# Performance work log

Hardware: AMD Instinct MI355X
Metric: run time of the kernel (lower is better)

Reference implementation:

```python
import jax, jax.numpy as jnp
import numpy as np

DIM = 128
H = 4            # num_heads
HD = DIM // H    # head_dim = 32
NH = H // 2      # half heads
MAXD = 128       # rpe max_dist
SPAN = 2 * MAXD + 1
TABLE = SPAN * SPAN
LAMBDA_INIT = 0.8


def setup_inputs() -> dict:
    key = jax.random.key(0)
    ks = jax.random.split(key, 18)
    B, Nq, Nkv = 2, 2048, 4096
    n = jax.random.normal
    inp = {
        "x_q": n(ks[0], (B, Nq, DIM), dtype=jnp.float32),
        "x_kv": n(ks[1], (B, Nkv, DIM), dtype=jnp.float32),
        "coords_q": jax.random.randint(ks[2], (B, Nq, 2), 0, 256, dtype=jnp.int32),
        "coords_k": jax.random.randint(ks[3], (B, Nkv, 2), 0, 256, dtype=jnp.int32),
        "alpha_map": jax.random.uniform(ks[4], (B, Nq, 1), dtype=jnp.float32),
        # projection weights stored input-major: y = x @ W + b
        "Wq": n(ks[5], (DIM, DIM), dtype=jnp.float32) * 0.02,
        "bq": jnp.zeros((DIM,), jnp.float32),
        "Wk": n(ks[6], (DIM, DIM), dtype=jnp.float32) * 0.02,
        "bk": jnp.zeros((DIM,), jnp.float32),
        "Wv": n(ks[7], (DIM, DIM), dtype=jnp.float32) * 0.02,
        "bv": jnp.zeros((DIM,), jnp.float32),
        "lq1": n(ks[8], (NH, HD), dtype=jnp.float32) * 0.1,
        "lk1": n(ks[9], (NH, HD), dtype=jnp.float32) * 0.1,
        "lq2": n(ks[10], (NH, HD), dtype=jnp.float32) * 0.1,
        "lk2": n(ks[11], (NH, HD), dtype=jnp.float32) * 0.1,
        "rpe_table": n(ks[12], (TABLE, H), dtype=jnp.float32) * 0.02,
        "Wp": n(ks[13], (DIM, DIM), dtype=jnp.float32) * 0.02,
        "bp": jnp.zeros((DIM,), jnp.float32),
    }
    return inp


def reference(x_q, x_kv, coords_q, coords_k, alpha_map,
              Wq, bq, Wk, bk, Wv, bv,
              lq1, lk1, lq2, lk2, rpe_table, Wp, bp):
    B, Nq, C = x_q.shape
    Nkv = x_kv.shape[1]
    scale = HD ** -0.5

    def to_heads(x, W, b, n):
        return (x @ W + b).reshape(B, n, H, HD).transpose(0, 2, 1, 3)  # [B,H,n,hd]

    q = to_heads(x_q, Wq, bq, Nq)
    k = to_heads(x_kv, Wk, bk, Nkv)
    v = to_heads(x_kv, Wv, bv, Nkv)

    # relative position bias gather: [B,Nq,Nkv] indices into [TABLE,H]
    rel = coords_q[:, :, None, :] - coords_k[:, None, :, :] + MAXD
    rel = jnp.clip(rel, 0, 2 * MAXD)
    idx = rel[..., 0] * SPAN + rel[..., 1]
    bias = jnp.transpose(rpe_table[idx], (0, 3, 1, 2))  # [B,H,Nq,Nkv]

    scores = jnp.einsum('bhqd,bhkd->bhqk', q, k) * scale + bias
    probs = jax.nn.softmax(scores, axis=-1)
    x_std = jnp.einsum('bhqk,bhkd->bhqd', probs, v)

    lam = (jnp.exp(jnp.sum(lq1 * lk1, axis=-1))
           - jnp.exp(jnp.sum(lq2 * lk2, axis=-1)) + LAMBDA_INIT)  # [NH]
    attn_diff = probs[:, :NH] - lam[None, :, None, None] * probs[:, NH:]
    x_diff = jnp.einsum('bhqk,bhkd->bhqd', attn_diff, v[:, :NH])

    x1 = x_std[:, :NH] + alpha_map[:, None, :, :] * x_diff  # alpha gating
    x = jnp.concatenate([x1, x_std[:, NH:]], axis=1)        # [B,H,Nq,hd]
    x = x.transpose(0, 2, 1, 3).reshape(B, Nq, C)
    return x @ Wp + bp
```

## Files before the change

### kernel.cpp

```cpp
#include <hip/hip_runtime.h>
#include <hip/hip_bf16.h>

#define B_ 2
#define H_ 4
#define HD_ 32
#define NQ_ 2048
#define NKV_ 4096
#define DIM_ 128
#define SPAN_ 257
#define SCALE_ 0.17677669529663687f
#define LAMBDA_INIT_ 0.8f
#define DTHR 4.0f

typedef float f32x4 __attribute__((ext_vector_type(4)));
typedef short s16x4 __attribute__((ext_vector_type(4)));
typedef short s16x8 __attribute__((ext_vector_type(8)));
typedef int   i32x4 __attribute__((ext_vector_type(4)));
typedef float fl4   __attribute__((ext_vector_type(4)));

static __device__ __forceinline__ unsigned short f2bf(float f) {
  unsigned u = __float_as_uint(f);
  u += 0x7FFFu + ((u >> 16) & 1u);
  return (unsigned short)(u >> 16);
}
static __device__ __forceinline__ unsigned cvtpk(float lo, float hi) {
  unsigned r;
  asm("v_cvt_pk_bf16_f32 %0, %1, %2" : "=v"(r) : "v"(lo), "v"(hi));
  return r;
}

__global__ __launch_bounds__(128) void proj_q(const float* __restrict__ x,
    const float* __restrict__ W, const float* __restrict__ bias,
    unsigned short* __restrict__ out) {
  int row0 = blockIdx.x * 16;
  int b = row0 / NQ_, n0 = row0 % NQ_;
  __shared__ float xr[16][DIM_ + 1];
  int j = threadIdx.x;
#pragma unroll
  for (int r = 0; r < 16; ++r) xr[r][j] = x[(size_t)(row0 + r) * DIM_ + j];
  __syncthreads();
  float acc[16];
  float bb = bias[j];
#pragma unroll
  for (int r = 0; r < 16; ++r) acc[r] = bb;
#pragma unroll 4
  for (int i = 0; i < DIM_; ++i) {
    float w = W[i * DIM_ + j];
#pragma unroll
    for (int r = 0; r < 16; ++r) acc[r] = fmaf(xr[r][i], w, acc[r]);
  }
  int h = j >> 5, d = j & 31;
#pragma unroll
  for (int r = 0; r < 16; ++r)
    out[(((size_t)b * H_ + h) * NQ_ + n0 + r) * HD_ + d] = f2bf(acc[r]);
}

__global__ __launch_bounds__(256) void proj_kv(const float* __restrict__ x,
    const float* __restrict__ Wk, const float* __restrict__ bk,
    const float* __restrict__ Wv, const float* __restrict__ bv,
    unsigned short* __restrict__ Kb, unsigned short* __restrict__ Vsw) {
  int row0 = blockIdx.x * 16;
  int b = row0 / NKV_, n0 = row0 % NKV_;
  __shared__ float xr[16][DIM_ + 1];
  int tid = threadIdx.x;
  int half = tid >> 7, j = tid & 127;
#pragma unroll
  for (int c = 0; c < 8; ++c) {
    int e = tid + c * 256;
    xr[e >> 7][e & 127] = x[(size_t)row0 * DIM_ + e];
  }
  __syncthreads();
  const float* W = half ? Wv : Wk;
  float bb = half ? bv[j] : bk[j];
  float acc[16];
#pragma unroll
  for (int r = 0; r < 16; ++r) acc[r] = bb;
#pragma unroll 4
  for (int i = 0; i < DIM_; ++i) {
    float w = W[i * DIM_ + j];
#pragma unroll
    for (int r = 0; r < 16; ++r) acc[r] = fmaf(xr[r][i], w, acc[r]);
  }
  int h = j >> 5, d = j & 31;
  if (half == 0) {
#pragma unroll
    for (int r = 0; r < 16; ++r)
      Kb[(((size_t)b * H_ + h) * NKV_ + n0 + r) * HD_ + d] = f2bf(acc[r]);
  } else {
    size_t vrow = (((size_t)b * H_ + h) * HD_ + d) * NKV_ + (size_t)(n0 & ~31);
#pragma unroll
    for (int c = 0; c < 4; ++c) {
      int k0r = (n0 & 31) + 4 * c;
      int posb = (k0r < 16) ? 8 * (k0r >> 2) : 8 * ((k0r - 16) >> 2) + 4;
      s16x4 t4;
#pragma unroll
      for (int e = 0; e < 4; ++e) t4[e] = (short)f2bf(acc[4 * c + e]);
      *(s16x4*)(Vsw + vrow + posb) = t4;
    }
  }
}

__global__ __launch_bounds__(128) void proj_out(const float* __restrict__ x,
    const float* __restrict__ W, const float* __restrict__ bias,
    float* __restrict__ out) {
  int row0 = blockIdx.x * 16;
  __shared__ float xr[16][DIM_ + 1];
  int j = threadIdx.x;
#pragma unroll
  for (int r = 0; r < 16; ++r) xr[r][j] = x[(size_t)(row0 + r) * DIM_ + j];
  __syncthreads();
  float acc[16];
  float bb = bias[j];
#pragma unroll
  for (int r = 0; r < 16; ++r) acc[r] = bb;
#pragma unroll 4
  for (int i = 0; i < DIM_; ++i) {
    float w = W[i * DIM_ + j];
#pragma unroll
    for (int r = 0; r < 16; ++r) acc[r] = fmaf(xr[r][i], w, acc[r]);
  }
#pragma unroll
  for (int r = 0; r < 16; ++r) out[(size_t)(row0 + r) * DIM_ + j] = acc[r];
}

__global__ __launch_bounds__(512) void attn_nb(
    const unsigned short* __restrict__ Qg, const unsigned short* __restrict__ Kg,
    const unsigned short* __restrict__ Vg, const int* __restrict__ cq,
    const int* __restrict__ ck, const float* __restrict__ alpha,
    const float* __restrict__ rpe, const float* __restrict__ lq1,
    const float* __restrict__ lk1, const float* __restrict__ lq2,
    const float* __restrict__ lk2, float* __restrict__ xatt) {

  const int tid = threadIdx.x;
  const int lane = tid & 63;
  const int wv = tid >> 6;
  const int qcol = lane & 15;
  const int g = lane >> 4;
  const int qt = blockIdx.x & 127;
  const int b = blockIdx.x >> 7;
  const int qg0 = qt * 16;
  const int k_base = wv * 512;

  __shared__ struct {
    float acc[3][8][16][36];
    float mW[8][17];
    float lW[4][8][17];
    float wgt[8][17];
    float lam[2];
  } S;

  if (tid < 2) {
    float s1 = 0.f, s2 = 0.f;
    for (int d = 0; d < HD_; ++d) {
      s1 += lq1[tid * HD_ + d] * lk1[tid * HD_ + d];
      s2 += lq2[tid * HD_ + d] * lk2[tid * HD_ + d];
    }
    S.lam[tid] = __expf(s1) - __expf(s2) + LAMBDA_INIT_;
  }

  s16x8 qf[4];
#pragma unroll
  for (int h = 0; h < 4; ++h)
    qf[h] = *(const s16x8*)(Qg + (((size_t)b * H_ + h) * NQ_ + qg0 + qcol) * HD_ + 8 * g);

  const int2 cqv = ((const int2*)cq)[(size_t)b * NQ_ + qg0 + qcol];
  const int qx = cqv.x + 128, qy = cqv.y + 128;

  const unsigned short* kb[4];
  const unsigned short* vp[4][2];
#pragma unroll
  for (int h = 0; h < 4; ++h) {
    kb[h] = Kg + (((size_t)b * H_ + h) * NKV_ + k_base) * HD_;
#pragma unroll
    for (int dt = 0; dt < 2; ++dt)
      vp[h][dt] = Vg + (((size_t)b * H_ + h) * HD_ + dt * 16 + qcol) * NKV_ + k_base + 8 * g;
  }
  int koff[2];
#pragma unroll
  for (int t = 0; t < 2; ++t) koff[t] = (16 * t + qcol) * HD_ + 8 * g;

  const i32x4* ck4 = (const i32x4*)ck + (((size_t)b * NKV_ + k_base) >> 1);
  const fl4* __restrict__ rpe4 = (const fl4*)rpe;

  float m_run = -INFINITY;
  float l_run[4] = {0.f, 0.f, 0.f, 0.f};
  f32x4 z4 = {0.f, 0.f, 0.f, 0.f};
  f32x4 aS[4][2], aC[2][2];
#pragma unroll
  for (int h = 0; h < 4; ++h) { aS[h][0] = z4; aS[h][1] = z4; }
#pragma unroll
  for (int p = 0; p < 2; ++p) { aC[p][0] = z4; aC[p][1] = z4; }

  s16x8 kf[4][2], vf[4][2];
  i32x4 ckt[4];
  fl4 gB[8];

#define CKLD(ST) {                                                         \
    const int s_ = (ST);                                                   \
    _Pragma("unroll") for (int t = 0; t < 2; ++t)                          \
    _Pragma("unroll") for (int hf = 0; hf < 2; ++hf)                       \
      ckt[2 * t + hf] = ck4[s_ * 16 + 8 * t + 2 * g + hf];                 \
  }
#define KLD(ST) {                                                          \
    const int s_ = (ST);                                                   \
    _Pragma("unroll") for (int h = 0; h < 4; ++h)                          \
    _Pragma("unroll") for (int t = 0; t < 2; ++t)                          \
      kf[h][t] = *(const s16x8*)(kb[h] + s_ * 32 * HD_ + koff[t]);         \
  }
#define VLD(ST) {                                                          \
    const int s_ = (ST);                                                   \
    _Pragma("unroll") for (int h = 0; h < 4; ++h)                          \
    _Pragma("unroll") for (int dt = 0; dt < 2; ++dt)                       \
      vf[h][dt] = *(const s16x8*)(vp[h][dt] + s_ * 32);                    \
  }
#define GATH() {                                                           \
    _Pragma("unroll") for (int t = 0; t < 2; ++t)                          \
    _Pragma("unroll") for (int hf = 0; hf < 2; ++hf) {                     \
      i32x4 cc = ckt[2 * t + hf];                                          \
      int dx0 = qx - cc[0]; dx0 = dx0 < 0 ? 0 : (dx0 > 256 ? 256 : dx0);   \
      int dy0 = qy - cc[1]; dy0 = dy0 < 0 ? 0 : (dy0 > 256 ? 256 : dy0);   \
      gB[4 * t + 2 * hf] = rpe4[dx0 * SPAN_ + dy0];                        \
      int dx1 = qx - cc[2]; dx1 = dx1 < 0 ? 0 : (dx1 > 256 ? 256 : dx1);   \
      int dy1 = qy - cc[3]; dy1 = dy1 < 0 ? 0 : (dy1 > 256 ? 256 : dy1);   \
      gB[4 * t + 2 * hf + 1] = rpe4[dx1 * SPAN_ + dy1];                    \
    }                                                                      \
  }

  CKLD(0);
  KLD(0);
  GATH();
  CKLD(1);

  for (int st = 0; st < 16; ++st) {
    f32x4 s0[4], s1[4];
#pragma unroll
    for (int h = 0; h < 4; ++h) {
      s0[h] = __builtin_amdgcn_mfma_f32_16x16x32_bf16(kf[h][0], qf[h], z4, 0, 0, 0);
      s1[h] = __builtin_amdgcn_mfma_f32_16x16x32_bf16(kf[h][1], qf[h], z4, 0, 0, 0);
    }
    VLD(st);
    KLD(st + 1 < 16 ? st + 1 : 15);

    float sv[4][8];
    float mx = -INFINITY;
#pragma unroll
    for (int h = 0; h < 4; ++h) {
#pragma unroll
      for (int r = 0; r < 4; ++r) {
        sv[h][r]     = fmaf(s0[h][r], SCALE_, gB[r][h]);
        sv[h][4 + r] = fmaf(s1[h][r], SCALE_, gB[4 + r][h]);
        mx = fmaxf(mx, fmaxf(sv[h][r], sv[h][4 + r]));
      }
    }
    mx = fmaxf(mx, __shfl_xor(mx, 16));
    mx = fmaxf(mx, __shfl_xor(mx, 32));
    if (__any(mx > m_run + DTHR)) {
      float mnew = fmaxf(m_run, mx);
      float fold = __expf(m_run - mnew);
      float fr[4];
#pragma unroll
      for (int r = 0; r < 4; ++r) fr[r] = __shfl(fold, 4 * g + r);
#pragma unroll
      for (int h = 0; h < 4; ++h) {
        l_run[h] *= fold;
#pragma unroll
        for (int dt = 0; dt < 2; ++dt)
#pragma unroll
          for (int r = 0; r < 4; ++r) aS[h][dt][r] *= fr[r];
      }
#pragma unroll
      for (int p = 0; p < 2; ++p)
#pragma unroll
        for (int dt = 0; dt < 2; ++dt)
#pragma unroll
          for (int r = 0; r < 4; ++r) aC[p][dt][r] *= fr[r];
      m_run = mnew;
    }
    s16x8 pa[4];
#pragma unroll
    for (int h = 0; h < 4; ++h) {
      float p[8], psum = 0.f;
#pragma unroll
      for (int s = 0; s < 8; ++s) { p[s] = __expf(sv[h][s] - m_run); psum += p[s]; }
      l_run[h] += psum;
      i32x4 pw;
#pragma unroll
      for (int c = 0; c < 4; ++c) pw[c] = (int)cvtpk(p[2 * c], p[2 * c + 1]);
      pa[h] = __builtin_bit_cast(s16x8, pw);
    }
    GATH();
    CKLD(st + 2 < 16 ? st + 2 : 15);

#pragma unroll
    for (int h = 0; h < 4; ++h)
#pragma unroll
      for (int dt = 0; dt < 2; ++dt)
        aS[h][dt] = __builtin_amdgcn_mfma_f32_16x16x32_bf16(pa[h], vf[h][dt], aS[h][dt], 0, 0, 0);
#pragma unroll
    for (int p = 0; p < 2; ++p)
#pragma unroll
      for (int dt = 0; dt < 2; ++dt)
        aC[p][dt] = __builtin_amdgcn_mfma_f32_16x16x32_bf16(pa[p + 2], vf[p][dt], aC[p][dt], 0, 0, 0);
  }

#pragma unroll
  for (int h = 0; h < 4; ++h) {
    l_run[h] += __shfl_xor(l_run[h], 16);
    l_run[h] += __shfl_xor(l_run[h], 32);
  }
  if (lane < 16) {
    S.mW[wv][lane] = m_run;
#pragma unroll
    for (int h = 0; h < 4; ++h) S.lW[h][wv][lane] = l_run[h];
  }
  __syncthreads();
  if (tid < 128) {
    int w = tid >> 4, q = tid & 15;
    float M = -INFINITY;
#pragma unroll
    for (int w2 = 0; w2 < 8; ++w2) M = fmaxf(M, S.mW[w2][q]);
    S.wgt[w][q] = __expf(S.mW[w][q] - M);
  }
  __syncthreads();

#pragma unroll
  for (int p = 0; p < 3; ++p)
#pragma unroll
    for (int dt = 0; dt < 2; ++dt)
#pragma unroll
      for (int r = 0; r < 4; ++r)
        S.acc[p][wv][4 * g + r][dt * 16 + qcol] = aS[p][dt][r];
  __syncthreads();
  const int q = tid >> 5, d = tid & 31;
  float wg[8];
#pragma unroll
  for (int w = 0; w < 8; ++w) wg[w] = S.wgt[w][q];
  float sumA[3] = {0.f, 0.f, 0.f};
#pragma unroll
  for (int p = 0; p < 3; ++p)
#pragma unroll
    for (int w = 0; w < 8; ++w) sumA[p] = fmaf(wg[w], S.acc[p][w][q][d], sumA[p]);
  __syncthreads();

#pragma unroll
  for (int dt = 0; dt < 2; ++dt)
#pragma unroll
    for (int r = 0; r < 4; ++r) {
      S.acc[0][wv][4 * g + r][dt * 16 + qcol] = aS[3][dt][r];
      S.acc[1][wv][4 * g + r][dt * 16 + qcol] = aC[0][dt][r];
      S.acc[2][wv][4 * g + r][dt * 16 + qcol] = aC[1][dt][r];
    }
  __syncthreads();
  float sumB[3] = {0.f, 0.f, 0.f};
#pragma unroll
  for (int p = 0; p < 3; ++p)
#pragma unroll
    for (int w = 0; w < 8; ++w) sumB[p] = fmaf(wg[w], S.acc[p][w][q][d], sumB[p]);

  float L[4];
#pragma unroll
  for (int h = 0; h < 4; ++h) {
    float s = 0.f;
#pragma unroll
    for (int w = 0; w < 8; ++w) s = fmaf(S.lW[h][w][q], wg[w], s);
    L[h] = s;
  }
  float a = alpha[(size_t)b * NQ_ + qg0 + q];
  float lam0 = S.lam[0], lam1 = S.lam[1];
  size_t ob = ((size_t)b * NQ_ + qg0 + q) * DIM_;
  xatt[ob + d]      = (1.f + a) * sumA[0] / L[0] - a * lam0 * sumB[1] / L[2];
  xatt[ob + 32 + d] = (1.f + a) * sumA[1] / L[1] - a * lam1 * sumB[2] / L[3];
  xatt[ob + 64 + d] = sumA[2] / L[2];
  xatt[ob + 96 + d] = sumB[0] / L[3];
}

extern "C" void kernel_launch(void* const* d_in, const int* in_sizes, int n_in,
                              void* d_out, int out_size, void* d_ws, size_t ws_size,
                              hipStream_t stream) {
  const float* x_q   = (const float*)d_in[0];
  const float* x_kv  = (const float*)d_in[1];
  const int*   cq    = (const int*)d_in[2];
  const int*   ckc   = (const int*)d_in[3];
  const float* alpha = (const float*)d_in[4];
  const float* Wq    = (const float*)d_in[5];
  const float* bq    = (const float*)d_in[6];
  const float* Wk    = (const float*)d_in[7];
  const float* bk    = (const float*)d_in[8];
  const float* Wv    = (const float*)d_in[9];
  const float* bv    = (const float*)d_in[10];
  const float* lq1   = (const float*)d_in[11];
  const float* lk1   = (const float*)d_in[12];
  const float* lq2   = (const float*)d_in[13];
  const float* lk2   = (const float*)d_in[14];
  const float* rpe   = (const float*)d_in[15];
  const float* Wp    = (const float*)d_in[16];
  const float* bp    = (const float*)d_in[17];
  float* out = (float*)d_out;

  char* w = (char*)d_ws;
  unsigned short* Qb  = (unsigned short*)w;
  unsigned short* Kb  = (unsigned short*)(w + 1048576);
  unsigned short* Vsw = (unsigned short*)(w + 3145728);
  float*          xat = (float*)(w + 5242880);

  proj_q<<<dim3(B_ * NQ_ / 16), dim3(128), 0, stream>>>(x_q, Wq, bq, Qb);
  proj_kv<<<dim3(B_ * NKV_ / 16), dim3(256), 0, stream>>>(x_kv, Wk, bk, Wv, bv, Kb, Vsw);

  attn_nb<<<dim3(B_ * (NQ_ / 16)), dim3(512), 0, stream>>>(
      Qb, Kb, Vsw, cq, ckc, alpha, rpe, lq1, lk1, lq2, lk2, xat);

  proj_out<<<dim3(B_ * NQ_ / 16), dim3(128), 0, stream>>>(xat, Wp, bp, out);
}
```

Before: 138.7 us.

## Merge Q/K/V projections into one launch and fuse output projection into attention

Combines the separate Q and KV projection kernels into a single launch that handles 32-row tiles, with wider float4 loads and 16-byte V stores. It also folds the output projection into the tail of the attention kernel, staging the 16x128 attention result in a shared-memory union and multiplying by Wp directly, which removes the xatt intermediate and one launch. The intent is to cut launch count and global round-trips of the intermediate activations. The cost is extra serial FMA work at the end of each attention block, and more register pressure in the 32-row KV projection.

```diff
diff --git a/kernel.cpp b/kernel.cpp
--- a/kernel.cpp
+++ b/kernel.cpp
@@ -29,98 +29,78 @@
   return r;
 }
 
-__global__ __launch_bounds__(128) void proj_q(const float* __restrict__ x,
-    const float* __restrict__ W, const float* __restrict__ bias,
-    unsigned short* __restrict__ out) {
-  int row0 = blockIdx.x * 16;
-  int b = row0 / NQ_, n0 = row0 % NQ_;
-  __shared__ float xr[16][DIM_ + 1];
-  int j = threadIdx.x;
-#pragma unroll
-  for (int r = 0; r < 16; ++r) xr[r][j] = x[(size_t)(row0 + r) * DIM_ + j];
-  __syncthreads();
-  float acc[16];
-  float bb = bias[j];
-#pragma unroll
-  for (int r = 0; r < 16; ++r) acc[r] = bb;
-#pragma unroll 4
-  for (int i = 0; i < DIM_; ++i) {
-    float w = W[i * DIM_ + j];
-#pragma unroll
-    for (int r = 0; r < 16; ++r) acc[r] = fmaf(xr[r][i], w, acc[r]);
-  }
-  int h = j >> 5, d = j & 31;
-#pragma unroll
-  for (int r = 0; r < 16; ++r)
-    out[(((size_t)b * H_ + h) * NQ_ + n0 + r) * HD_ + d] = f2bf(acc[r]);
-}
-
-__global__ __launch_bounds__(256) void proj_kv(const float* __restrict__ x,
+__global__ __launch_bounds__(256) void qkv_proj(
+    const float* __restrict__ xq, const float* __restrict__ xkv,
+    const float* __restrict__ Wq, const float* __restrict__ bq,
     const float* __restrict__ Wk, const float* __restrict__ bk,
     const float* __restrict__ Wv, const float* __restrict__ bv,
-    unsigned short* __restrict__ Kb, unsigned short* __restrict__ Vsw) {
-  int row0 = blockIdx.x * 16;
-  int b = row0 / NKV_, n0 = row0 % NKV_;
-  __shared__ float xr[16][DIM_ + 1];
-  int tid = threadIdx.x;
-  int half = tid >> 7, j = tid & 127;
-#pragma unroll
-  for (int c = 0; c < 8; ++c) {
-    int e = tid + c * 256;
-    xr[e >> 7][e & 127] = x[(size_t)row0 * DIM_ + e];
-  }
-  __syncthreads();
-  const float* W = half ? Wv : Wk;
-  float bb = half ? bv[j] : bk[j];
-  float acc[16];
-#pragma unroll
-  for (int r = 0; r < 16; ++r) acc[r] = bb;
+    unsigned short* __restrict__ Qb, unsigned short* __restrict__ Kb,
+    unsigned short* __restrict__ Vsw) {
+  const int idx = blockIdx.x;
+  const int b = idx / 192, r = idx % 192;
+  const bool isq = r < 64;
+  const int row0 = isq ? r * 32 : (r - 64) * 32;
+  const int nlen = isq ? NQ_ : NKV_;
+  const float* xsrc = isq ? xq : xkv;
+
+  __shared__ __align__(16) float xr[32][DIM_];
+  const int tid = threadIdx.x;
+  const float* xbase = xsrc + ((size_t)b * nlen + row0) * DIM_;
+#pragma unroll
+  for (int c = 0; c < 4; ++c) {
+    int id = tid + c * 256;
+    int rr = id >> 5, c4 = id & 31;
+    *(fl4*)&xr[rr][c4 * 4] = *(const fl4*)(xbase + rr * DIM_ + c4 * 4);
+  }
+  __syncthreads();
+
+  if (isq) {
+    const int j = tid & 127, rh = tid >> 7;
+    float acc[16];
+    float bb = bq[j];
+#pragma unroll
+    for (int rr = 0; rr < 16; ++rr) acc[rr] = bb;
 #pragma unroll 4
-  for (int i = 0; i < DIM_; ++i) {
-    float w = W[i * DIM_ + j];
-#pragma unroll
-    for (int r = 0; r < 16; ++r) acc[r] = fmaf(xr[r][i], w, acc[r]);
-  }
-  int h = j >> 5, d = j & 31;
-  if (half == 0) {
-#pragma unroll
-    for (int r = 0; r < 16; ++r)
-      Kb[(((size_t)b * H_ + h) * NKV_ + n0 + r) * HD_ + d] = f2bf(acc[r]);
+    for (int i = 0; i < DIM_; ++i) {
+      float w = Wq[i * DIM_ + j];
+#pragma unroll
+      for (int rr = 0; rr < 16; ++rr) acc[rr] = fmaf(xr[16 * rh + rr][i], w, acc[rr]);
+    }
+    int h = j >> 5, d = j & 31;
+    unsigned short* qb = Qb + (((size_t)b * H_ + h) * NQ_ + row0 + 16 * rh) * HD_ + d;
+#pragma unroll
+    for (int rr = 0; rr < 16; ++rr) qb[rr * HD_] = f2bf(acc[rr]);
   } else {
-    size_t vrow = (((size_t)b * H_ + h) * HD_ + d) * NKV_ + (size_t)(n0 & ~31);
-#pragma unroll
-    for (int c = 0; c < 4; ++c) {
-      int k0r = (n0 & 31) + 4 * c;
-      int posb = (k0r < 16) ? 8 * (k0r >> 2) : 8 * ((k0r - 16) >> 2) + 4;
-      s16x4 t4;
-#pragma unroll
-      for (int e = 0; e < 4; ++e) t4[e] = (short)f2bf(acc[4 * c + e]);
-      *(s16x4*)(Vsw + vrow + posb) = t4;
-    }
-  }
-}
-
-__global__ __launch_bounds__(128) void proj_out(const float* __restrict__ x,
-    const float* __restrict__ W, const float* __restrict__ bias,
-    float* __restrict__ out) {
-  int row0 = blockIdx.x * 16;
-  __shared__ float xr[16][DIM_ + 1];
-  int j = threadIdx.x;
-#pragma unroll
-  for (int r = 0; r < 16; ++r) xr[r][j] = x[(size_t)(row0 + r) * DIM_ + j];
-  __syncthreads();
-  float acc[16];
-  float bb = bias[j];
-#pragma unroll
-  for (int r = 0; r < 16; ++r) acc[r] = bb;
-#pragma unroll 4
-  for (int i = 0; i < DIM_; ++i) {
-    float w = W[i * DIM_ + j];
-#pragma unroll
-    for (int r = 0; r < 16; ++r) acc[r] = fmaf(xr[r][i], w, acc[r]);
-  }
-#pragma unroll
-  for (int r = 0; r < 16; ++r) out[(size_t)(row0 + r) * DIM_ + j] = acc[r];
+    const int half = tid >> 7, j = tid & 127;
+    const float* W = half ? Wv : Wk;
+    float bb = half ? bv[j] : bk[j];
+    float acc[32];
+#pragma unroll
+    for (int rr = 0; rr < 32; ++rr) acc[rr] = bb;
+#pragma unroll 2
+    for (int i = 0; i < DIM_; ++i) {
+      float w = W[i * DIM_ + j];
+#pragma unroll
+      for (int rr = 0; rr < 32; ++rr) acc[rr] = fmaf(xr[rr][i], w, acc[rr]);
+    }
+    int h = j >> 5, d = j & 31;
+    if (half == 0) {
+      unsigned short* kb2 = Kb + (((size_t)b * H_ + h) * NKV_ + row0) * HD_ + d;
+#pragma unroll
+      for (int rr = 0; rr < 32; ++rr) kb2[rr * HD_] = f2bf(acc[rr]);
+    } else {
+      unsigned short* vb = Vsw + (((size_t)b * H_ + h) * HD_ + d) * NKV_ + row0;
+#pragma unroll
+      for (int g = 0; g < 4; ++g) {
+        s16x8 t;
+#pragma unroll
+        for (int j0 = 0; j0 < 4; ++j0) t[j0] = (short)f2bf(acc[4 * g + j0]);
+#pragma unroll
+        for (int j0 = 4; j0 < 8; ++j0) t[j0] = (short)f2bf(acc[16 + 4 * g + (j0 - 4)]);
+        *(s16x8*)(vb + 8 * g) = t;
+      }
+    }
+  }
 }
 
 __global__ __launch_bounds__(512) void attn_nb(
@@ -129,7 +109,8 @@
     const int* __restrict__ ck, const float* __restrict__ alpha,
     const float* __restrict__ rpe, const float* __restrict__ lq1,
     const float* __restrict__ lk1, const float* __restrict__ lq2,
-    const float* __restrict__ lk2, float* __restrict__ xatt) {
+    const float* __restrict__ lk2, const float* __restrict__ Wp,
+    const float* __restrict__ bp, float* __restrict__ out) {
 
   const int tid = threadIdx.x;
   const int lane = tid & 63;
@@ -142,7 +123,10 @@
   const int k_base = wv * 512;
 
   __shared__ struct {
-    float acc[3][8][16][36];
+    union {
+      float acc[3][8][16][36];
+      float xq[16][128];
+    } u;
     float mW[8][17];
     float lW[4][8][17];
     float wgt[8][17];
@@ -329,7 +313,7 @@
     for (int dt = 0; dt < 2; ++dt)
 #pragma unroll
       for (int r = 0; r < 4; ++r)
-        S.acc[p][wv][4 * g + r][dt * 16 + qcol] = aS[p][dt][r];
+        S.u.acc[p][wv][4 * g + r][dt * 16 + qcol] = aS[p][dt][r];
   __syncthreads();
   const int q = tid >> 5, d = tid & 31;
   float wg[8];
@@ -339,23 +323,23 @@
 #pragma unroll
   for (int p = 0; p < 3; ++p)
 #pragma unroll
-    for (int w = 0; w < 8; ++w) sumA[p] = fmaf(wg[w], S.acc[p][w][q][d], sumA[p]);
+    for (int w = 0; w < 8; ++w) sumA[p] = fmaf(wg[w], S.u.acc[p][w][q][d], sumA[p]);
   __syncthreads();
 
 #pragma unroll
   for (int dt = 0; dt < 2; ++dt)
 #pragma unroll
     for (int r = 0; r < 4; ++r) {
-      S.acc[0][wv][4 * g + r][dt * 16 + qcol] = aS[3][dt][r];
-      S.acc[1][wv][4 * g + r][dt * 16 + qcol] = aC[0][dt][r];
-      S.acc[2][wv][4 * g + r][dt * 16 + qcol] = aC[1][dt][r];
+      S.u.acc[0][wv][4 * g + r][dt * 16 + qcol] = aS[3][dt][r];
+      S.u.acc[1][wv][4 * g + r][dt * 16 + qcol] = aC[0][dt][r];
+      S.u.acc[2][wv][4 * g + r][dt * 16 + qcol] = aC[1][dt][r];
     }
   __syncthreads();
   float sumB[3] = {0.f, 0.f, 0.f};
 #pragma unroll
   for (int p = 0; p < 3; ++p)
 #pragma unroll
-    for (int w = 0; w < 8; ++w) sumB[p] = fmaf(wg[w], S.acc[p][w][q][d], sumB[p]);
+    for (int w = 0; w < 8; ++w) sumB[p] = fmaf(wg[w], S.u.acc[p][w][q][d], sumB[p]);
 
   float L[4];
 #pragma unroll
@@ -367,11 +351,34 @@
   }
   float a = alpha[(size_t)b * NQ_ + qg0 + q];
   float lam0 = S.lam[0], lam1 = S.lam[1];
-  size_t ob = ((size_t)b * NQ_ + qg0 + q) * DIM_;
-  xatt[ob + d]      = (1.f + a) * sumA[0] / L[0] - a * lam0 * sumB[1] / L[2];
-  xatt[ob + 32 + d] = (1.f + a) * sumA[1] / L[1] - a * lam1 * sumB[2] / L[3];
-  xatt[ob + 64 + d] = sumA[2] / L[2];
-  xatt[ob + 96 + d] = sumB[0] / L[3];
+  float xv0 = (1.f + a) * sumA[0] / L[0] - a * lam0 * sumB[1] / L[2];
+  float xv1 = (1.f + a) * sumA[1] / L[1] - a * lam1 * sumB[2] / L[3];
+  float xv2 = sumA[2] / L[2];
+  float xv3 = sumB[0] / L[3];
+
+  __syncthreads();
+  S.u.xq[q][d]      = xv0;
+  S.u.xq[q][32 + d] = xv1;
+  S.u.xq[q][64 + d] = xv2;
+  S.u.xq[q][96 + d] = xv3;
+  __syncthreads();
+
+  {
+    const int j = tid & 127, rg = tid >> 7;
+    float ob[4];
+    float bpj = bp[j];
+#pragma unroll
+    for (int rr = 0; rr < 4; ++rr) ob[rr] = bpj;
+#pragma unroll 4
+    for (int i = 0; i < DIM_; ++i) {
+      float w = Wp[i * DIM_ + j];
+#pragma unroll
+      for (int rr = 0; rr < 4; ++rr) ob[rr] = fmaf(S.u.xq[4 * rg + rr][i], w, ob[rr]);
+    }
+#pragma unroll
+    for (int rr = 0; rr < 4; ++rr)
+      out[((size_t)b * NQ_ + qg0 + 4 * rg + rr) * DIM_ + j] = ob[rr];
+  }
 }
 
 extern "C" void kernel_launch(void* const* d_in, const int* in_sizes, int n_in,
@@ -401,13 +408,10 @@
   unsigned short* Qb  = (unsigned short*)w;
   unsigned short* Kb  = (unsigned short*)(w + 1048576);
   unsigned short* Vsw = (unsigned short*)(w + 3145728);
-  float*          xat = (float*)(w + 5242880);
-
-  proj_q<<<dim3(B_ * NQ_ / 16), dim3(128), 0, stream>>>(x_q, Wq, bq, Qb);
-  proj_kv<<<dim3(B_ * NKV_ / 16), dim3(256), 0, stream>>>(x_kv, Wk, bk, Wv, bv, Kb, Vsw);
+
+  qkv_proj<<<dim3(B_ * 192), dim3(256), 0, stream>>>(
+      x_q, x_kv, Wq, bq, Wk, bk, Wv, bv, Qb, Kb, Vsw);
 
   attn_nb<<<dim3(B_ * (NQ_ / 16)), dim3(512), 0, stream>>>(
-      Qb, Kb, Vsw, cq, ckc, alpha, rpe, lq1, lk1, lq2, lk2, xat);
-
-  proj_out<<<dim3(B_ * NQ_ / 16), dim3(128), 0, stream>>>(xat, Wp, bp, out);
+      Qb, Kb, Vsw, cq, ckc, alpha, rpe, lq1, lk1, lq2, lk2, Wp, bp, out);
 }
```

Result: faster. 131.6 us (-5.1%).
